# Optimization experiments

Hardware: AMD Instinct MI355X
Metric: run time of the kernel (lower is better)

The kernel has to match this reference:

```python
import jax, jax.numpy as jnp
import numpy as np

EPS = 1e-12


def _segment_softmax(logits, seg, n):
    # numerically stable softmax over edges grouped by destination node
    m = jax.ops.segment_max(logits, seg, num_segments=n)
    e = jnp.exp(logits - m[seg])
    s = jax.ops.segment_sum(e, seg, num_segments=n)
    return e / s[seg]


def _agnn(x, src, dst, beta, n):
    # cosine-similarity attention (PyG AGNNConv): alpha_ij = softmax_i(beta * <x_i/|x_i|, x_j/|x_j|>)
    norm = jnp.sqrt(jnp.sum(x * x, axis=-1, keepdims=True))
    xn = x / jnp.maximum(norm, EPS)
    logits = beta * jnp.sum(xn[dst] * xn[src], axis=-1)  # [E+N]
    alpha = _segment_softmax(logits, dst, n)
    return jax.ops.segment_sum(alpha[:, None] * x[src], dst, num_segments=n)


def setup_inputs() -> dict:
    key = jax.random.key(0)
    ks = jax.random.split(key, 6)
    N, E, F, H, C = 100000, 3200000, 512, 16, 7
    x = jax.random.normal(ks[0], (N, F), dtype=jnp.float32)
    edge_index = jax.random.randint(ks[1], (2, E), 0, N, dtype=jnp.int32)
    W1 = jax.random.normal(ks[2], (H, F), dtype=jnp.float32) * 0.05
    b1 = jnp.zeros((H,), jnp.float32)
    W2 = jax.random.normal(ks[3], (C, H), dtype=jnp.float32) * 0.2
    b2 = jnp.zeros((C,), jnp.float32)
    return {
        "x": x, "edge_index": edge_index,
        "W1": W1, "b1": b1,
        "beta2": jnp.ones((1,), jnp.float32),
        "beta3": jnp.ones((1,), jnp.float32),
        "beta4": jnp.ones((1,), jnp.float32),
        "W2": W2, "b2": b2,
    }


def reference(x, edge_index, W1, b1, beta2, beta3, beta4, W2, b2):
    N = x.shape[0]
    loop = jnp.arange(N, dtype=edge_index.dtype)
    src = jnp.concatenate([edge_index[0], loop])  # self-loops added by AGNNConv
    dst = jnp.concatenate([edge_index[1], loop])

    h = jax.nn.relu(x @ W1.T + b1)                 # lin1 on raw features (eval: dropout = id)
    h = _agnn(h, src, dst, jnp.float32(1.0), N)    # prop1: beta fixed at 1 (requires_grad=False)
    h = _agnn(h, src, dst, beta2[0], N)
    h = _agnn(h, src, dst, beta3[0], N)
    h = _agnn(h, src, dst, beta4[0], N)
    logits = h @ W2.T + b2
    return jax.nn.log_softmax(logits, axis=1)
```

## Files before the change

kernel.cpp:

```cpp
#include <hip/hip_runtime.h>
#include <hip/hip_fp16.h>
#include <math.h>

#define F 512
#define H 16
#define C 7
#define NB 512
#define BIN_CHUNK 4096

typedef _Float16 h2 __attribute__((ext_vector_type(2)));

__device__ __forceinline__ h2 as_h2(unsigned u) { return __builtin_bit_cast(h2, u); }
__device__ __forceinline__ unsigned as_u32(h2 v) { return __builtin_bit_cast(unsigned, v); }

__device__ __forceinline__ float dot2acc(h2 a, h2 b, float c) {
#if __has_builtin(__builtin_amdgcn_fdot2)
    return __builtin_amdgcn_fdot2(a, b, c, false);
#else
    return c + (float)a[0] * (float)b[0] + (float)a[1] * (float)b[1];
#endif
}

__global__ void zero_i32(int* p, int n) {
    int i = blockIdx.x * blockDim.x + threadIdx.x;
    if (i < n) p[i] = 0;
}

__global__ __launch_bounds__(256) void bin_edges(const int* __restrict__ ei, int E, int Etot,
                                                 int width, int cap, int* __restrict__ gcnt,
                                                 unsigned* __restrict__ binned) {
    __shared__ int cnt[NB];
    __shared__ int base[NB];
    int t = threadIdx.x;
    for (int i = t; i < NB; i += 256) cnt[i] = 0;
    __syncthreads();
    long chunk0 = (long)blockIdx.x * BIN_CHUNK;
    for (int k = 0; k < BIN_CHUNK / 256; ++k) {
        long e = chunk0 + k * 256 + t;
        if (e < Etot) {
            int dst = (e < E) ? ei[E + e] : (int)(e - E);
            atomicAdd(&cnt[dst / width], 1);
        }
    }
    __syncthreads();
    for (int i = t; i < NB; i += 256) {
        int c = cnt[i];
        base[i] = c ? atomicAdd(&gcnt[i], c) : 0;
        cnt[i] = 0;
    }
    __syncthreads();
    for (int k = 0; k < BIN_CHUNK / 256; ++k) {
        long e = chunk0 + k * 256 + t;
        if (e < Etot) {
            int src, dst;
            if (e < E) { src = ei[e]; dst = ei[E + e]; }
            else       { src = (int)(e - E); dst = src; }
            int b = dst / width;
            size_t pos = (size_t)b * cap + base[b] + atomicAdd(&cnt[b], 1);
            binned[pos] = (unsigned)src | ((unsigned)(dst - b * width) << 17);
        }
    }
}

__global__ void bucket_scan(const int* __restrict__ gcnt, int Etot,
                            int* __restrict__ bbase, int* __restrict__ rp, int N) {
    __shared__ int s[NB];
    int t = threadIdx.x;
    int own = gcnt[t];
    s[t] = own;
    __syncthreads();
    for (int d = 1; d < NB; d <<= 1) {
        int add = (t >= d) ? s[t - d] : 0;
        __syncthreads();
        s[t] += add;
        __syncthreads();
    }
    bbase[t] = s[t] - own;
    if (t == NB - 1) bbase[NB] = s[t];
    if (t == 0) rp[N] = Etot;
}

__global__ __launch_bounds__(256) void bucket_sort(const unsigned* __restrict__ binned,
                                                   const int* __restrict__ gcnt,
                                                   const int* __restrict__ bbase,
                                                   int width, int cap, int N,
                                                   int* __restrict__ rp, int* __restrict__ srcs) {
    __shared__ int cnt[256];
    __shared__ int cur[256];
    int b = blockIdx.x, t = threadIdx.x;
    int r0 = bbase[b];
    int ne = gcnt[b];
    const unsigned* bin = binned + (size_t)b * cap;
    int nodeBase = b * width;
    cnt[t] = 0;
    cur[t] = 0;
    __syncthreads();
    for (int e = t; e < ne; e += 256) {
        atomicAdd(&cnt[bin[e] >> 17], 1);
    }
    __syncthreads();
    int own = cnt[t];
    for (int d = 1; d < 256; d <<= 1) {
        int add = (t >= d) ? cnt[t - d] : 0;
        __syncthreads();
        cnt[t] += add;
        __syncthreads();
    }
    int excl = cnt[t] - own;
    int node = nodeBase + t;
    if (t < width && node < N) rp[node] = r0 + excl;
    __syncthreads();
    cnt[t] = excl;
    __syncthreads();
    for (int e = t; e < ne; e += 256) {
        unsigned p = bin[e];
        int dL = p >> 17;
        int pos = r0 + cnt[dL] + atomicAdd(&cur[dL], 1);
        srcs[pos] = (int)(p & 0x1FFFFu);
    }
}

__global__ __launch_bounds__(256) void lin1_relu(const float* __restrict__ x,
                                                 const float* __restrict__ W1,
                                                 const float* __restrict__ b1,
                                                 __half* __restrict__ hrow, int N) {
    __shared__ float4 w4[16 * 16 * 9];
    int t = threadIdx.x;
    for (int r = 0; r < 8; ++r) {
        int idx = r * 256 + t;
        int j = idx >> 7;
        int rem = idx & 127;
        int s = rem >> 3, m = rem & 7;
        w4[(j * 16 + s) * 9 + m] = ((const float4*)W1)[idx];
    }
    __syncthreads();

    int s = t & 15, g = t >> 4;
    int iA = blockIdx.x * 32 + g;
    int iB = iA + 16;
    int iAc = min(iA, N - 1), iBc = min(iB, N - 1);

    const float4* xA4 = (const float4*)(x + (size_t)iAc * F);
    const float4* xB4 = (const float4*)(x + (size_t)iBc * F);
    float4 xa[8], xb[8];
#pragma unroll
    for (int m = 0; m < 8; ++m) xa[m] = xA4[s * 8 + m];
#pragma unroll
    for (int m = 0; m < 8; ++m) xb[m] = xB4[s * 8 + m];

    float vA[16], vB[16];
#pragma unroll
    for (int j = 0; j < 16; ++j) { vA[j] = 0.f; vB[j] = 0.f; }
#pragma unroll
    for (int j = 0; j < 16; ++j) {
        const float4* wr = &w4[(j * 16 + s) * 9];
#pragma unroll
        for (int m = 0; m < 8; ++m) {
            float4 w = wr[m];
            vA[j] += w.x * xa[m].x + w.y * xa[m].y + w.z * xa[m].z + w.w * xa[m].w;
            vB[j] += w.x * xb[m].x + w.y * xb[m].y + w.z * xb[m].z + w.w * xb[m].w;
        }
    }

#pragma unroll
    for (int st = 0; st < 4; ++st) {
        int bit = (s >> st) & 1;
        int cntj = 16 >> (st + 1);
#pragma unroll
        for (int k = 0; k < 8; ++k) {
            if (k < cntj) {
                float keepA = bit ? vA[2 * k + 1] : vA[2 * k];
                float giveA = bit ? vA[2 * k] : vA[2 * k + 1];
                vA[k] = keepA + __shfl_xor(giveA, 1 << st);
                float keepB = bit ? vB[2 * k + 1] : vB[2 * k];
                float giveB = bit ? vB[2 * k] : vB[2 * k + 1];
                vB[k] = keepB + __shfl_xor(giveB, 1 << st);
            }
        }
    }

    float bs = b1[s];
    float oA = fmaxf(vA[0] + bs, 0.f);
    float oB = fmaxf(vB[0] + bs, 0.f);

    float sqA = oA * oA, sqB = oB * oB;
    sqA += __shfl_xor(sqA, 1); sqA += __shfl_xor(sqA, 2);
    sqA += __shfl_xor(sqA, 4); sqA += __shfl_xor(sqA, 8);
    sqB += __shfl_xor(sqB, 1); sqB += __shfl_xor(sqB, 2);
    sqB += __shfl_xor(sqB, 4); sqB += __shfl_xor(sqB, 8);
    float rnA = 1.0f / fmaxf(sqrtf(sqA), 1e-12f);
    float rnB = 1.0f / fmaxf(sqrtf(sqB), 1e-12f);

    if (iA < N) {
        hrow[(size_t)iA * 32 + s] = __float2half(oA * rnA);
        hrow[(size_t)iA * 32 + 16 + s] = __float2half(oA);
    }
    if (iB < N) {
        hrow[(size_t)iB * 32 + s] = __float2half(oB * rnB);
        hrow[(size_t)iB * 32 + 16 + s] = __float2half(oB);
    }
}

__global__ __launch_bounds__(256) void agnn_step(const uint4* __restrict__ hrow,
                                                 const int* __restrict__ rp,
                                                 const int* __restrict__ srcs,
                                                 const float* __restrict__ bp,
                                                 uint4* __restrict__ hrow_out, int N) {
    int t = threadIdx.x;
    int sub = t & 3, g = t >> 2;
    int i = blockIdx.x * 64 + g;
    if (i >= N) return;

    const float L2E = 1.4426950408889634f;
    float beta = bp ? bp[0] : 1.0f;
    float aL = beta * L2E;
    float mm = fabsf(beta) * L2E;

    uint4 hA = hrow[(size_t)i * 4 + 0];
    uint4 hB = hrow[(size_t)i * 4 + 1];
    h2 hi[8];
    hi[0] = as_h2(hA.x); hi[1] = as_h2(hA.y); hi[2] = as_h2(hA.z); hi[3] = as_h2(hA.w);
    hi[4] = as_h2(hB.x); hi[5] = as_h2(hB.y); hi[6] = as_h2(hB.z); hi[7] = as_h2(hB.w);

    int e0 = rp[i];
    int deg = rp[i + 1] - e0;
    int dm1 = deg - 1;
    int U = (deg + 3) >> 2;

    int sbuf[4];
    uint4 rbuf[4][4];
#pragma unroll
    for (int u = 0; u < 4; ++u) {
        int s = srcs[e0 + min(sub + 4 * u, dm1)];
        const uint4* r = hrow + (size_t)s * 4;
        rbuf[u][0] = r[0]; rbuf[u][1] = r[1]; rbuf[u][2] = r[2]; rbuf[u][3] = r[3];
        sbuf[u] = srcs[e0 + min(sub + 4 * (u + 4), dm1)];
    }

    float denom = 0.f;
    float acc[16];
#pragma unroll
    for (int j = 0; j < 16; ++j) acc[j] = 0.f;

    for (int mb = 0; mb < U; mb += 4) {
#pragma unroll
        for (int u = 0; u < 4; ++u) {
            int m = mb + u;
            int k = sub + 4 * m;
            uint4 a = rbuf[u][0], b = rbuf[u][1], c = rbuf[u][2], d = rbuf[u][3];
            int snext = sbuf[u];
            sbuf[u] = srcs[e0 + min(sub + 4 * (m + 8), dm1)];
            const uint4* r = hrow + (size_t)snext * 4;
            rbuf[u][0] = r[0]; rbuf[u][1] = r[1]; rbuf[u][2] = r[2]; rbuf[u][3] = r[3];

            float dot = 0.f;
            dot = dot2acc(hi[0], as_h2(a.x), dot);
            dot = dot2acc(hi[1], as_h2(a.y), dot);
            dot = dot2acc(hi[2], as_h2(a.z), dot);
            dot = dot2acc(hi[3], as_h2(a.w), dot);
            dot = dot2acc(hi[4], as_h2(b.x), dot);
            dot = dot2acc(hi[5], as_h2(b.y), dot);
            dot = dot2acc(hi[6], as_h2(b.z), dot);
            dot = dot2acc(hi[7], as_h2(b.w), dot);

            float w = exp2f(fmaf(aL, dot, -mm));
            w = (k < deg) ? w : 0.f;
            denom += w;

            h2 c0 = as_h2(c.x), c1 = as_h2(c.y), c2 = as_h2(c.z), c3 = as_h2(c.w);
            h2 d0 = as_h2(d.x), d1 = as_h2(d.y), d2 = as_h2(d.z), d3 = as_h2(d.w);
            acc[0]  = fmaf(w, (float)c0[0], acc[0]);
            acc[1]  = fmaf(w, (float)c0[1], acc[1]);
            acc[2]  = fmaf(w, (float)c1[0], acc[2]);
            acc[3]  = fmaf(w, (float)c1[1], acc[3]);
            acc[4]  = fmaf(w, (float)c2[0], acc[4]);
            acc[5]  = fmaf(w, (float)c2[1], acc[5]);
            acc[6]  = fmaf(w, (float)c3[0], acc[6]);
            acc[7]  = fmaf(w, (float)c3[1], acc[7]);
            acc[8]  = fmaf(w, (float)d0[0], acc[8]);
            acc[9]  = fmaf(w, (float)d0[1], acc[9]);
            acc[10] = fmaf(w, (float)d1[0], acc[10]);
            acc[11] = fmaf(w, (float)d1[1], acc[11]);
            acc[12] = fmaf(w, (float)d2[0], acc[12]);
            acc[13] = fmaf(w, (float)d2[1], acc[13]);
            acc[14] = fmaf(w, (float)d3[0], acc[14]);
            acc[15] = fmaf(w, (float)d3[1], acc[15]);
        }
    }

    denom += __shfl_xor(denom, 1);
    denom += __shfl_xor(denom, 2);
#pragma unroll
    for (int j = 0; j < 16; ++j) {
        acc[j] += __shfl_xor(acc[j], 1);
        acc[j] += __shfl_xor(acc[j], 2);
    }

    float rd = 1.0f / denom;
    float o[16];
    float sq = 0.f;
#pragma unroll
    for (int j = 0; j < 16; ++j) {
        o[j] = acc[j] * rd;
        sq = fmaf(o[j], o[j], sq);
    }
    float rno = 1.0f / fmaxf(sqrtf(sq), 1e-12f);

    float scale = (sub < 2) ? rno : 1.0f;
    int half = (sub & 1) * 8;
    uint4 wq;
    {
        h2 t0, t1;
        t0[0] = (_Float16)(o[half + 0] * scale); t0[1] = (_Float16)(o[half + 1] * scale);
        t1[0] = (_Float16)(o[half + 2] * scale); t1[1] = (_Float16)(o[half + 3] * scale);
        wq.x = as_u32(t0); wq.y = as_u32(t1);
        t0[0] = (_Float16)(o[half + 4] * scale); t0[1] = (_Float16)(o[half + 5] * scale);
        t1[0] = (_Float16)(o[half + 6] * scale); t1[1] = (_Float16)(o[half + 7] * scale);
        wq.z = as_u32(t0); wq.w = as_u32(t1);
    }
    hrow_out[(size_t)i * 4 + sub] = wq;
}

__global__ __launch_bounds__(256) void head_kernel(const uint4* __restrict__ hrow,
                                                   const float* __restrict__ W2,
                                                   const float* __restrict__ b2,
                                                   float* __restrict__ out, int N) {
    __shared__ float w2[C * H];
    __shared__ float bb[C];
    int t = threadIdx.x;
    if (t < C * H) w2[t] = W2[t];
    if (t < C) bb[t] = b2[t];
    __syncthreads();
    int i = blockIdx.x * blockDim.x + t;
    if (i >= N) return;
    uint4 cA = hrow[(size_t)i * 4 + 2];
    uint4 cB = hrow[(size_t)i * 4 + 3];
    float hv[H];
    {
        h2 v;
        v = as_h2(cA.x); hv[0] = (float)v[0];  hv[1] = (float)v[1];
        v = as_h2(cA.y); hv[2] = (float)v[0];  hv[3] = (float)v[1];
        v = as_h2(cA.z); hv[4] = (float)v[0];  hv[5] = (float)v[1];
        v = as_h2(cA.w); hv[6] = (float)v[0];  hv[7] = (float)v[1];
        v = as_h2(cB.x); hv[8] = (float)v[0];  hv[9] = (float)v[1];
        v = as_h2(cB.y); hv[10] = (float)v[0]; hv[11] = (float)v[1];
        v = as_h2(cB.z); hv[12] = (float)v[0]; hv[13] = (float)v[1];
        v = as_h2(cB.w); hv[14] = (float)v[0]; hv[15] = (float)v[1];
    }
    float lg[C];
    float m = -1e30f;
#pragma unroll
    for (int c = 0; c < C; ++c) {
        float s = bb[c];
#pragma unroll
        for (int k = 0; k < H; ++k) s += hv[k] * w2[c * H + k];
        lg[c] = s;
        m = fmaxf(m, s);
    }
    float sum = 0.f;
#pragma unroll
    for (int c = 0; c < C; ++c) sum += expf(lg[c] - m);
    float lse = m + logf(sum);
    float* op = out + (size_t)i * C;
#pragma unroll
    for (int c = 0; c < C; ++c) op[c] = lg[c] - lse;
}

extern "C" void kernel_launch(void* const* d_in, const int* in_sizes, int n_in,
                              void* d_out, int out_size, void* d_ws, size_t ws_size,
                              hipStream_t stream) {
    const float* x     = (const float*)d_in[0];
    const int*   ei    = (const int*)d_in[1];
    const float* W1    = (const float*)d_in[2];
    const float* b1    = (const float*)d_in[3];
    const float* beta2 = (const float*)d_in[4];
    const float* beta3 = (const float*)d_in[5];
    const float* beta4 = (const float*)d_in[6];
    const float* W2    = (const float*)d_in[7];
    const float* b2    = (const float*)d_in[8];
    float* out = (float*)d_out;

    int N = in_sizes[0] / F;
    int E = in_sizes[1] / 2;
    int Etot = E + N;
    int width = (N + NB - 1) / NB;
    int cap = (Etot / NB) * 5 / 4;

    char* p = (char*)d_ws;
    uint4* hr_a = (uint4*)p; p += (size_t)N * 64;
    uint4* hr_b = (uint4*)p; p += (size_t)N * 64;
    int* rp     = (int*)p;   p += (size_t)(N + 1) * 4;
    int* srcs   = (int*)p;   p += (size_t)Etot * 4;
    int* gcnt   = (int*)p;   p += (size_t)NB * 4;
    int* bbase  = (int*)p;   p += (size_t)(NB + 1) * 4;
    p = (char*)(((size_t)p + 255) & ~(size_t)255);
    unsigned* binned = (unsigned*)p; p += (size_t)NB * cap * 4;

    zero_i32<<<(NB + 255) / 256, 256, 0, stream>>>(gcnt, NB);
    bin_edges<<<(Etot + BIN_CHUNK - 1) / BIN_CHUNK, 256, 0, stream>>>(ei, E, Etot, width, cap, gcnt, binned);
    bucket_scan<<<1, NB, 0, stream>>>(gcnt, Etot, bbase, rp, N);
    bucket_sort<<<NB, 256, 0, stream>>>(binned, gcnt, bbase, width, cap, N, rp, srcs);

    lin1_relu<<<(N + 31) / 32, 256, 0, stream>>>(x, W1, b1, (__half*)hr_a, N);

    int gs = (N + 63) / 64;
    agnn_step<<<gs, 256, 0, stream>>>(hr_a, rp, srcs, nullptr, hr_b, N);
    agnn_step<<<gs, 256, 0, stream>>>(hr_b, rp, srcs, beta2, hr_a, N);
    agnn_step<<<gs, 256, 0, stream>>>(hr_a, rp, srcs, beta3, hr_b, N);
    agnn_step<<<gs, 256, 0, stream>>>(hr_b, rp, srcs, beta4, hr_a, N);

    head_kernel<<<(N + 255) / 256, 256, 0, stream>>>(hr_a, W2, b2, out, N);
}
```

Baseline: 603.2 us.

## Store normalized features plus scalar norm instead of both raw and normalized rows

Each node row previously held both the normalized and raw 16-dim half vectors (64 bytes). It now stores only the normalized vector (32 bytes) plus a separate float norm, and rebuilds the raw features as norm times normalized inside the aggregation and the head. This roughly halves the bytes gathered per edge in the memory-bound agnn_step. The cost is an extra scattered 4-byte norm load per edge and a small change in rounding from reconstructing raw values out of fp16 normalized values.

After: 645.2 us. 1.07x slower.

```diff
diff --git a/kernel.cpp b/kernel.cpp
--- a/kernel.cpp
+++ b/kernel.cpp
@@ -123,7 +123,8 @@
 __global__ __launch_bounds__(256) void lin1_relu(const float* __restrict__ x,
                                                  const float* __restrict__ W1,
                                                  const float* __restrict__ b1,
-                                                 __half* __restrict__ hrow, int N) {
+                                                 __half* __restrict__ hnrow,
+                                                 float* __restrict__ nrm, int N) {
     __shared__ float4 w4[16 * 16 * 9];
     int t = threadIdx.x;
     for (int r = 0; r < 8; ++r) {
@@ -188,24 +189,27 @@
     sqA += __shfl_xor(sqA, 4); sqA += __shfl_xor(sqA, 8);
     sqB += __shfl_xor(sqB, 1); sqB += __shfl_xor(sqB, 2);
     sqB += __shfl_xor(sqB, 4); sqB += __shfl_xor(sqB, 8);
-    float rnA = 1.0f / fmaxf(sqrtf(sqA), 1e-12f);
-    float rnB = 1.0f / fmaxf(sqrtf(sqB), 1e-12f);
+    float nA = sqrtf(sqA), nB = sqrtf(sqB);
+    float rnA = 1.0f / fmaxf(nA, 1e-12f);
+    float rnB = 1.0f / fmaxf(nB, 1e-12f);
 
     if (iA < N) {
-        hrow[(size_t)iA * 32 + s] = __float2half(oA * rnA);
-        hrow[(size_t)iA * 32 + 16 + s] = __float2half(oA);
+        hnrow[(size_t)iA * 16 + s] = __float2half(oA * rnA);
+        if (s == 0) nrm[iA] = nA;
     }
     if (iB < N) {
-        hrow[(size_t)iB * 32 + s] = __float2half(oB * rnB);
-        hrow[(size_t)iB * 32 + 16 + s] = __float2half(oB);
-    }
-}
-
-__global__ __launch_bounds__(256) void agnn_step(const uint4* __restrict__ hrow,
+        hnrow[(size_t)iB * 16 + s] = __float2half(oB * rnB);
+        if (s == 0) nrm[iB] = nB;
+    }
+}
+
+__global__ __launch_bounds__(256) void agnn_step(const uint4* __restrict__ hn,
+                                                 const float* __restrict__ nv,
                                                  const int* __restrict__ rp,
                                                  const int* __restrict__ srcs,
                                                  const float* __restrict__ bp,
-                                                 uint4* __restrict__ hrow_out, int N) {
+                                                 uint4* __restrict__ hn_out,
+                                                 float* __restrict__ nv_out, int N) {
     int t = threadIdx.x;
     int sub = t & 3, g = t >> 2;
     int i = blockIdx.x * 64 + g;
@@ -216,8 +220,8 @@
     float aL = beta * L2E;
     float mm = fabsf(beta) * L2E;
 
-    uint4 hA = hrow[(size_t)i * 4 + 0];
-    uint4 hB = hrow[(size_t)i * 4 + 1];
+    uint4 hA = hn[(size_t)i * 2 + 0];
+    uint4 hB = hn[(size_t)i * 2 + 1];
     h2 hi[8];
     hi[0] = as_h2(hA.x); hi[1] = as_h2(hA.y); hi[2] = as_h2(hA.z); hi[3] = as_h2(hA.w);
     hi[4] = as_h2(hB.x); hi[5] = as_h2(hB.y); hi[6] = as_h2(hB.z); hi[7] = as_h2(hB.w);
@@ -228,12 +232,14 @@
     int U = (deg + 3) >> 2;
 
     int sbuf[4];
-    uint4 rbuf[4][4];
+    uint4 rb0[4], rb1[4];
+    float nb[4];
 #pragma unroll
     for (int u = 0; u < 4; ++u) {
         int s = srcs[e0 + min(sub + 4 * u, dm1)];
-        const uint4* r = hrow + (size_t)s * 4;
-        rbuf[u][0] = r[0]; rbuf[u][1] = r[1]; rbuf[u][2] = r[2]; rbuf[u][3] = r[3];
+        const uint4* r = hn + (size_t)s * 2;
+        rb0[u] = r[0]; rb1[u] = r[1];
+        nb[u] = nv[s];
         sbuf[u] = srcs[e0 + min(sub + 4 * (u + 4), dm1)];
     }
 
@@ -247,11 +253,13 @@
         for (int u = 0; u < 4; ++u) {
             int m = mb + u;
             int k = sub + 4 * m;
-            uint4 a = rbuf[u][0], b = rbuf[u][1], c = rbuf[u][2], d = rbuf[u][3];
+            uint4 a = rb0[u], b = rb1[u];
+            float nn = nb[u];
             int snext = sbuf[u];
             sbuf[u] = srcs[e0 + min(sub + 4 * (m + 8), dm1)];
-            const uint4* r = hrow + (size_t)snext * 4;
-            rbuf[u][0] = r[0]; rbuf[u][1] = r[1]; rbuf[u][2] = r[2]; rbuf[u][3] = r[3];
+            const uint4* r = hn + (size_t)snext * 2;
+            rb0[u] = r[0]; rb1[u] = r[1];
+            nb[u] = nv[snext];
 
             float dot = 0.f;
             dot = dot2acc(hi[0], as_h2(a.x), dot);
@@ -266,25 +274,26 @@
             float w = exp2f(fmaf(aL, dot, -mm));
             w = (k < deg) ? w : 0.f;
             denom += w;
-
-            h2 c0 = as_h2(c.x), c1 = as_h2(c.y), c2 = as_h2(c.z), c3 = as_h2(c.w);
-            h2 d0 = as_h2(d.x), d1 = as_h2(d.y), d2 = as_h2(d.z), d3 = as_h2(d.w);
-            acc[0]  = fmaf(w, (float)c0[0], acc[0]);
-            acc[1]  = fmaf(w, (float)c0[1], acc[1]);
-            acc[2]  = fmaf(w, (float)c1[0], acc[2]);
-            acc[3]  = fmaf(w, (float)c1[1], acc[3]);
-            acc[4]  = fmaf(w, (float)c2[0], acc[4]);
-            acc[5]  = fmaf(w, (float)c2[1], acc[5]);
-            acc[6]  = fmaf(w, (float)c3[0], acc[6]);
-            acc[7]  = fmaf(w, (float)c3[1], acc[7]);
-            acc[8]  = fmaf(w, (float)d0[0], acc[8]);
-            acc[9]  = fmaf(w, (float)d0[1], acc[9]);
-            acc[10] = fmaf(w, (float)d1[0], acc[10]);
-            acc[11] = fmaf(w, (float)d1[1], acc[11]);
-            acc[12] = fmaf(w, (float)d2[0], acc[12]);
-            acc[13] = fmaf(w, (float)d2[1], acc[13]);
-            acc[14] = fmaf(w, (float)d3[0], acc[14]);
-            acc[15] = fmaf(w, (float)d3[1], acc[15]);
+            float wn = w * nn;
+
+            h2 a0 = as_h2(a.x), a1 = as_h2(a.y), a2 = as_h2(a.z), a3 = as_h2(a.w);
+            h2 b0 = as_h2(b.x), b1h = as_h2(b.y), b2h = as_h2(b.z), b3 = as_h2(b.w);
+            acc[0]  = fmaf(wn, (float)a0[0], acc[0]);
+            acc[1]  = fmaf(wn, (float)a0[1], acc[1]);
+            acc[2]  = fmaf(wn, (float)a1[0], acc[2]);
+            acc[3]  = fmaf(wn, (float)a1[1], acc[3]);
+            acc[4]  = fmaf(wn, (float)a2[0], acc[4]);
+            acc[5]  = fmaf(wn, (float)a2[1], acc[5]);
+            acc[6]  = fmaf(wn, (float)a3[0], acc[6]);
+            acc[7]  = fmaf(wn, (float)a3[1], acc[7]);
+            acc[8]  = fmaf(wn, (float)b0[0], acc[8]);
+            acc[9]  = fmaf(wn, (float)b0[1], acc[9]);
+            acc[10] = fmaf(wn, (float)b1h[0], acc[10]);
+            acc[11] = fmaf(wn, (float)b1h[1], acc[11]);
+            acc[12] = fmaf(wn, (float)b2h[0], acc[12]);
+            acc[13] = fmaf(wn, (float)b2h[1], acc[13]);
+            acc[14] = fmaf(wn, (float)b3[0], acc[14]);
+            acc[15] = fmaf(wn, (float)b3[1], acc[15]);
         }
     }
 
@@ -304,24 +313,27 @@
         o[j] = acc[j] * rd;
         sq = fmaf(o[j], o[j], sq);
     }
-    float rno = 1.0f / fmaxf(sqrtf(sq), 1e-12f);
-
-    float scale = (sub < 2) ? rno : 1.0f;
-    int half = (sub & 1) * 8;
-    uint4 wq;
-    {
+    float no = sqrtf(sq);
+    float rno = 1.0f / fmaxf(no, 1e-12f);
+
+    if (sub < 2) {
+        int half = sub * 8;
+        uint4 wq;
         h2 t0, t1;
-        t0[0] = (_Float16)(o[half + 0] * scale); t0[1] = (_Float16)(o[half + 1] * scale);
-        t1[0] = (_Float16)(o[half + 2] * scale); t1[1] = (_Float16)(o[half + 3] * scale);
+        t0[0] = (_Float16)(o[half + 0] * rno); t0[1] = (_Float16)(o[half + 1] * rno);
+        t1[0] = (_Float16)(o[half + 2] * rno); t1[1] = (_Float16)(o[half + 3] * rno);
         wq.x = as_u32(t0); wq.y = as_u32(t1);
-        t0[0] = (_Float16)(o[half + 4] * scale); t0[1] = (_Float16)(o[half + 5] * scale);
-        t1[0] = (_Float16)(o[half + 6] * scale); t1[1] = (_Float16)(o[half + 7] * scale);
+        t0[0] = (_Float16)(o[half + 4] * rno); t0[1] = (_Float16)(o[half + 5] * rno);
+        t1[0] = (_Float16)(o[half + 6] * rno); t1[1] = (_Float16)(o[half + 7] * rno);
         wq.z = as_u32(t0); wq.w = as_u32(t1);
-    }
-    hrow_out[(size_t)i * 4 + sub] = wq;
-}
-
-__global__ __launch_bounds__(256) void head_kernel(const uint4* __restrict__ hrow,
+        hn_out[(size_t)i * 2 + sub] = wq;
+    } else if (sub == 2) {
+        nv_out[i] = no;
+    }
+}
+
+__global__ __launch_bounds__(256) void head_kernel(const uint4* __restrict__ hn,
+                                                   const float* __restrict__ nv,
                                                    const float* __restrict__ W2,
                                                    const float* __restrict__ b2,
                                                    float* __restrict__ out, int N) {
@@ -333,19 +345,20 @@
     __syncthreads();
     int i = blockIdx.x * blockDim.x + t;
     if (i >= N) return;
-    uint4 cA = hrow[(size_t)i * 4 + 2];
-    uint4 cB = hrow[(size_t)i * 4 + 3];
+    uint4 cA = hn[(size_t)i * 2 + 0];
+    uint4 cB = hn[(size_t)i * 2 + 1];
+    float nm = nv[i];
     float hv[H];
     {
         h2 v;
-        v = as_h2(cA.x); hv[0] = (float)v[0];  hv[1] = (float)v[1];
-        v = as_h2(cA.y); hv[2] = (float)v[0];  hv[3] = (float)v[1];
-        v = as_h2(cA.z); hv[4] = (float)v[0];  hv[5] = (float)v[1];
-        v = as_h2(cA.w); hv[6] = (float)v[0];  hv[7] = (float)v[1];
-        v = as_h2(cB.x); hv[8] = (float)v[0];  hv[9] = (float)v[1];
-        v = as_h2(cB.y); hv[10] = (float)v[0]; hv[11] = (float)v[1];
-        v = as_h2(cB.z); hv[12] = (float)v[0]; hv[13] = (float)v[1];
-        v = as_h2(cB.w); hv[14] = (float)v[0]; hv[15] = (float)v[1];
+        v = as_h2(cA.x); hv[0] = (float)v[0] * nm;  hv[1] = (float)v[1] * nm;
+        v = as_h2(cA.y); hv[2] = (float)v[0] * nm;  hv[3] = (float)v[1] * nm;
+        v = as_h2(cA.z); hv[4] = (float)v[0] * nm;  hv[5] = (float)v[1] * nm;
+        v = as_h2(cA.w); hv[6] = (float)v[0] * nm;  hv[7] = (float)v[1] * nm;
+        v = as_h2(cB.x); hv[8] = (float)v[0] * nm;  hv[9] = (float)v[1] * nm;
+        v = as_h2(cB.y); hv[10] = (float)v[0] * nm; hv[11] = (float)v[1] * nm;
+        v = as_h2(cB.z); hv[12] = (float)v[0] * nm; hv[13] = (float)v[1] * nm;
+        v = as_h2(cB.w); hv[14] = (float)v[0] * nm; hv[15] = (float)v[1] * nm;
     }
     float lg[C];
     float m = -1e30f;
@@ -387,8 +400,10 @@
     int cap = (Etot / NB) * 5 / 4;
 
     char* p = (char*)d_ws;
-    uint4* hr_a = (uint4*)p; p += (size_t)N * 64;
-    uint4* hr_b = (uint4*)p; p += (size_t)N * 64;
+    uint4* hn_a = (uint4*)p; p += (size_t)N * 32;
+    uint4* hn_b = (uint4*)p; p += (size_t)N * 32;
+    float* nv_a = (float*)p; p += (size_t)N * 4;
+    float* nv_b = (float*)p; p += (size_t)N * 4;
     int* rp     = (int*)p;   p += (size_t)(N + 1) * 4;
     int* srcs   = (int*)p;   p += (size_t)Etot * 4;
     int* gcnt   = (int*)p;   p += (size_t)NB * 4;
@@ -401,13 +416,13 @@
     bucket_scan<<<1, NB, 0, stream>>>(gcnt, Etot, bbase, rp, N);
     bucket_sort<<<NB, 256, 0, stream>>>(binned, gcnt, bbase, width, cap, N, rp, srcs);
 
-    lin1_relu<<<(N + 31) / 32, 256, 0, stream>>>(x, W1, b1, (__half*)hr_a, N);
+    lin1_relu<<<(N + 31) / 32, 256, 0, stream>>>(x, W1, b1, (__half*)hn_a, nv_a, N);
 
     int gs = (N + 63) / 64;
-    agnn_step<<<gs, 256, 0, stream>>>(hr_a, rp, srcs, nullptr, hr_b, N);
-    agnn_step<<<gs, 256, 0, stream>>>(hr_b, rp, srcs, beta2, hr_a, N);
-    agnn_step<<<gs, 256, 0, stream>>>(hr_a, rp, srcs, beta3, hr_b, N);
-    agnn_step<<<gs, 256, 0, stream>>>(hr_b, rp, srcs, beta4, hr_a, N);
-
-    head_kernel<<<(N + 255) / 256, 256, 0, stream>>>(hr_a, W2, b2, out, N);
-}
+    agnn_step<<<gs, 256, 0, stream>>>(hn_a, nv_a, rp, srcs, nullptr, hn_b, nv_b, N);
+    agnn_step<<<gs, 256, 0, stream>>>(hn_b, nv_b, rp, srcs, beta2, hn_a, nv_a, N);
+    agnn_step<<<gs, 256, 0, stream>>>(hn_a, nv_a, rp, srcs, beta3, hn_b, nv_b, N);
+    agnn_step<<<gs, 256, 0, stream>>>(hn_b, nv_b, rp, srcs, beta4, hn_a, nv_a, N);
+
+    head_kernel<<<(N + 255) / 256, 256, 0, stream>>>(hn_a, nv_a, W2, b2, out, N);
+}
```

## Replace two-level bucket sort CSR build with global atomic counting sort

Applied to the files above, without the earlier changes.

Swaps the binned two-pass bucket sort (shared-memory binning into 512 buckets, then per-bucket local sort) for a plain counting sort. Per-node degrees are counted with global atomics, a three-kernel prefix scan builds row pointers, and edges are scattered with per-node global atomic cursors. This drops the intermediate binned buffer and its extra read/write pass, but relies on many contended global atomics and random scattered writes. Edge order within a row becomes nondeterministic.

Result: slower. 911.0 us (+51.0%).

```diff
diff --git a/kernel.cpp b/kernel.cpp
--- a/kernel.cpp
+++ b/kernel.cpp
@@ -5,8 +5,6 @@
 #define F 512
 #define H 16
 #define C 7
-#define NB 512
-#define BIN_CHUNK 4096
 
 typedef _Float16 h2 __attribute__((ext_vector_type(2)));
 
@@ -26,97 +24,94 @@
     if (i < n) p[i] = 0;
 }
 
-__global__ __launch_bounds__(256) void bin_edges(const int* __restrict__ ei, int E, int Etot,
-                                                 int width, int cap, int* __restrict__ gcnt,
-                                                 unsigned* __restrict__ binned) {
-    __shared__ int cnt[NB];
-    __shared__ int base[NB];
-    int t = threadIdx.x;
-    for (int i = t; i < NB; i += 256) cnt[i] = 0;
+__global__ __launch_bounds__(256) void count_edges(const int* __restrict__ ei, int E, int Etot,
+                                                   int* __restrict__ rp) {
+    int stride = gridDim.x * blockDim.x;
+    for (int e = blockIdx.x * blockDim.x + threadIdx.x; e < Etot; e += stride) {
+        int dst = (e < E) ? ei[E + e] : (e - E);
+        atomicAdd(&rp[dst + 1], 1);
+    }
+}
+
+__global__ __launch_bounds__(256) void scan_chunk(int* __restrict__ rp, int n,
+                                                  int* __restrict__ bsum) {
+    __shared__ int s[256];
+    int b = blockIdx.x, t = threadIdx.x;
+    int base = b * 1024 + t * 4;
+    int v0 = 0, v1 = 0, v2 = 0, v3 = 0;
+    if (base + 3 < n) {
+        int4 q = *(const int4*)(rp + base);
+        v0 = q.x; v1 = q.y; v2 = q.z; v3 = q.w;
+    } else {
+        if (base < n)     v0 = rp[base];
+        if (base + 1 < n) v1 = rp[base + 1];
+        if (base + 2 < n) v2 = rp[base + 2];
+        if (base + 3 < n) v3 = rp[base + 3];
+    }
+    v1 += v0; v2 += v1; v3 += v2;
+    s[t] = v3;
     __syncthreads();
-    long chunk0 = (long)blockIdx.x * BIN_CHUNK;
-    for (int k = 0; k < BIN_CHUNK / 256; ++k) {
-        long e = chunk0 + k * 256 + t;
-        if (e < Etot) {
-            int dst = (e < E) ? ei[E + e] : (int)(e - E);
-            atomicAdd(&cnt[dst / width], 1);
-        }
-    }
-    __syncthreads();
-    for (int i = t; i < NB; i += 256) {
-        int c = cnt[i];
-        base[i] = c ? atomicAdd(&gcnt[i], c) : 0;
-        cnt[i] = 0;
-    }
-    __syncthreads();
-    for (int k = 0; k < BIN_CHUNK / 256; ++k) {
-        long e = chunk0 + k * 256 + t;
-        if (e < Etot) {
-            int src, dst;
-            if (e < E) { src = ei[e]; dst = ei[E + e]; }
-            else       { src = (int)(e - E); dst = src; }
-            int b = dst / width;
-            size_t pos = (size_t)b * cap + base[b] + atomicAdd(&cnt[b], 1);
-            binned[pos] = (unsigned)src | ((unsigned)(dst - b * width) << 17);
-        }
-    }
-}
-
-__global__ void bucket_scan(const int* __restrict__ gcnt, int Etot,
-                            int* __restrict__ bbase, int* __restrict__ rp, int N) {
-    __shared__ int s[NB];
-    int t = threadIdx.x;
-    int own = gcnt[t];
-    s[t] = own;
-    __syncthreads();
-    for (int d = 1; d < NB; d <<= 1) {
+    for (int d = 1; d < 256; d <<= 1) {
         int add = (t >= d) ? s[t - d] : 0;
         __syncthreads();
         s[t] += add;
         __syncthreads();
     }
-    bbase[t] = s[t] - own;
-    if (t == NB - 1) bbase[NB] = s[t];
-    if (t == 0) rp[N] = Etot;
-}
-
-__global__ __launch_bounds__(256) void bucket_sort(const unsigned* __restrict__ binned,
-                                                   const int* __restrict__ gcnt,
-                                                   const int* __restrict__ bbase,
-                                                   int width, int cap, int N,
-                                                   int* __restrict__ rp, int* __restrict__ srcs) {
-    __shared__ int cnt[256];
-    __shared__ int cur[256];
+    int excl = s[t] - v3;
+    v0 += excl; v1 += excl; v2 += excl; v3 += excl;
+    if (base + 3 < n) {
+        int4 q; q.x = v0; q.y = v1; q.z = v2; q.w = v3;
+        *(int4*)(rp + base) = q;
+    } else {
+        if (base < n)     rp[base] = v0;
+        if (base + 1 < n) rp[base + 1] = v1;
+        if (base + 2 < n) rp[base + 2] = v2;
+        if (base + 3 < n) rp[base + 3] = v3;
+    }
+    if (t == 255) bsum[b] = s[255];
+}
+
+__global__ void scan_top(int* __restrict__ bsum, int nb) {
+    __shared__ int s[128];
+    int t = threadIdx.x;
+    int v = (t < nb) ? bsum[t] : 0;
+    s[t] = v;
+    __syncthreads();
+    for (int d = 1; d < 128; d <<= 1) {
+        int a = (t >= d) ? s[t - d] : 0;
+        __syncthreads();
+        s[t] += a;
+        __syncthreads();
+    }
+    if (t < nb) bsum[t] = s[t] - v;
+}
+
+__global__ __launch_bounds__(256) void scan_add(int* __restrict__ rp, int n,
+                                                const int* __restrict__ bsum,
+                                                int* __restrict__ cur, int N) {
     int b = blockIdx.x, t = threadIdx.x;
-    int r0 = bbase[b];
-    int ne = gcnt[b];
-    const unsigned* bin = binned + (size_t)b * cap;
-    int nodeBase = b * width;
-    cnt[t] = 0;
-    cur[t] = 0;
-    __syncthreads();
-    for (int e = t; e < ne; e += 256) {
-        atomicAdd(&cnt[bin[e] >> 17], 1);
-    }
-    __syncthreads();
-    int own = cnt[t];
-    for (int d = 1; d < 256; d <<= 1) {
-        int add = (t >= d) ? cnt[t - d] : 0;
-        __syncthreads();
-        cnt[t] += add;
-        __syncthreads();
-    }
-    int excl = cnt[t] - own;
-    int node = nodeBase + t;
-    if (t < width && node < N) rp[node] = r0 + excl;
-    __syncthreads();
-    cnt[t] = excl;
-    __syncthreads();
-    for (int e = t; e < ne; e += 256) {
-        unsigned p = bin[e];
-        int dL = p >> 17;
-        int pos = r0 + cnt[dL] + atomicAdd(&cur[dL], 1);
-        srcs[pos] = (int)(p & 0x1FFFFu);
+    int add = bsum[b];
+    int base = b * 1024 + t * 4;
+#pragma unroll
+    for (int k = 0; k < 4; ++k) {
+        int idx = base + k;
+        if (idx < n) {
+            int v = rp[idx] + add;
+            if (add) rp[idx] = v;
+            if (idx < N) cur[idx] = v;
+        }
+    }
+}
+
+__global__ __launch_bounds__(256) void place_edges(const int* __restrict__ ei, int E, int Etot,
+                                                   int* __restrict__ cur, int* __restrict__ srcs) {
+    int stride = gridDim.x * blockDim.x;
+    for (int e = blockIdx.x * blockDim.x + threadIdx.x; e < Etot; e += stride) {
+        int src, dst;
+        if (e < E) { src = ei[e]; dst = ei[E + e]; }
+        else       { src = e - E; dst = src; }
+        int pos = atomicAdd(&cur[dst], 1);
+        srcs[pos] = src;
     }
 }
 
@@ -383,23 +378,23 @@
     int N = in_sizes[0] / F;
     int E = in_sizes[1] / 2;
     int Etot = E + N;
-    int width = (N + NB - 1) / NB;
-    int cap = (Etot / NB) * 5 / 4;
 
     char* p = (char*)d_ws;
     uint4* hr_a = (uint4*)p; p += (size_t)N * 64;
     uint4* hr_b = (uint4*)p; p += (size_t)N * 64;
     int* rp     = (int*)p;   p += (size_t)(N + 1) * 4;
+    int* cur    = (int*)p;   p += (size_t)N * 4;
     int* srcs   = (int*)p;   p += (size_t)Etot * 4;
-    int* gcnt   = (int*)p;   p += (size_t)NB * 4;
-    int* bbase  = (int*)p;   p += (size_t)(NB + 1) * 4;
-    p = (char*)(((size_t)p + 255) & ~(size_t)255);
-    unsigned* binned = (unsigned*)p; p += (size_t)NB * cap * 4;
-
-    zero_i32<<<(NB + 255) / 256, 256, 0, stream>>>(gcnt, NB);
-    bin_edges<<<(Etot + BIN_CHUNK - 1) / BIN_CHUNK, 256, 0, stream>>>(ei, E, Etot, width, cap, gcnt, binned);
-    bucket_scan<<<1, NB, 0, stream>>>(gcnt, Etot, bbase, rp, N);
-    bucket_sort<<<NB, 256, 0, stream>>>(binned, gcnt, bbase, width, cap, N, rp, srcs);
+    int* bsum   = (int*)p;   p += (size_t)128 * 4;
+
+    int nb = (N + 1 + 1023) / 1024;
+
+    zero_i32<<<(N + 1 + 255) / 256, 256, 0, stream>>>(rp, N + 1);
+    count_edges<<<2048, 256, 0, stream>>>(ei, E, Etot, rp);
+    scan_chunk<<<nb, 256, 0, stream>>>(rp, N + 1, bsum);
+    scan_top<<<1, 128, 0, stream>>>(bsum, nb);
+    scan_add<<<nb, 256, 0, stream>>>(rp, N + 1, bsum, cur, N);
+    place_edges<<<2048, 256, 0, stream>>>(ei, E, Etot, cur, srcs);
 
     lin1_relu<<<(N + 31) / 32, 256, 0, stream>>>(x, W1, b1, (__half*)hr_a, N);
 
```
